# Performance work log

Hardware: AMD Instinct MI355X
Metric: run time of the kernel (lower is better)

Reference implementation:

```python
import jax, jax.numpy as jnp
import numpy as np

B, S = 1, 2048
D = 2048            # n_embd
H = 16              # num heads
KV = 4              # num kv heads
GROUPS = H // KV
D_NOPE = 128
D_ROPE = 64
D_QK = D_NOPE + D_ROPE   # 192
D_V = 128
Q_RANK = 1536
KV_RANK = 512
EPS = 1e-6
MAX_POS = 4096


def rms_norm(x, w, eps=EPS):
    x32 = x.astype(jnp.float32)
    y = x32 * jax.lax.rsqrt(jnp.mean(x32 * x32, axis=-1, keepdims=True) + eps)
    return y.astype(x.dtype) * w


def rotate_half(x):
    x1, x2 = jnp.split(x, 2, axis=-1)
    return jnp.concatenate((-x2, x1), axis=-1)


def setup_inputs() -> dict:
    key = jax.random.key(0)
    ks = jax.random.split(key, 10)
    inv_freq = 1.0 / (10000.0 ** (jnp.arange(0, D_ROPE, 2, dtype=jnp.float32) / D_ROPE))
    t = jnp.arange(MAX_POS, dtype=jnp.float32)
    freqs = jnp.outer(t, inv_freq)                      # [MAX_POS, D_ROPE//2]
    emb = jnp.concatenate((freqs, freqs), axis=-1)      # [MAX_POS, D_ROPE]
    def lin(k, fan_in, fan_out):
        return jax.random.normal(k, (fan_in, fan_out), dtype=jnp.float32) * (fan_in ** -0.5)
    return {
        "hidden_states": jax.random.normal(ks[0], (B, S, D), dtype=jnp.float32),
        "cos": jnp.cos(emb)[None],                      # [1, MAX_POS, D_ROPE]
        "sin": jnp.sin(emb)[None],
        "wq_a": lin(ks[1], D, Q_RANK),
        "q_a_ln_w": jnp.ones((Q_RANK,), jnp.float32),
        "wq_b": lin(ks[2], Q_RANK, H * D_QK),
        "wkv_a": lin(ks[3], D, KV_RANK + D_ROPE),
        "kv_a_ln_w": jnp.ones((KV_RANK,), jnp.float32),
        "wkv_b": lin(ks[4], KV_RANK, KV * (D_NOPE + D_V)),
        "wo": lin(ks[5], H * D_V, D),
        "cache_position": jnp.arange(S, dtype=jnp.int64),
    }


def reference(hidden_states, cos, sin, wq_a, q_a_ln_w, wq_b, wkv_a, kv_a_ln_w,
              wkv_b, wo, cache_position):
    b, s, _ = hidden_states.shape
    # --- query low-rank path ---
    q_a = hidden_states @ wq_a                           # [B,S,Q_RANK]
    q = rms_norm(q_a, q_a_ln_w) @ wq_b                   # [B,S,H*D_QK]
    q = q.reshape(b, s, H, D_QK).transpose(0, 2, 1, 3)   # [B,H,S,D_QK]
    q_pass, q_rot = q[..., :D_NOPE], q[..., D_NOPE:]
    # --- kv low-rank path ---
    ckv = hidden_states @ wkv_a                          # [B,S,KV_RANK+D_ROPE]
    k_pass_a, k_rot_a = ckv[..., :KV_RANK], ckv[..., KV_RANK:]
    kv = rms_norm(k_pass_a, kv_a_ln_w) @ wkv_b           # [B,S,KV*(D_NOPE+D_V)]
    kv = kv.reshape(b, s, KV, D_NOPE + D_V).transpose(0, 2, 1, 3)  # [B,KV,S,*]
    k_pass, v = kv[..., :D_NOPE], kv[..., D_NOPE:]
    # --- partial RoPE ---
    c = cos[0][cache_position][None, None]               # [1,1,S,D_ROPE]
    sn = sin[0][cache_position][None, None]
    q_rot = q_rot * c + rotate_half(q_rot) * sn          # [B,H,S,D_ROPE]
    k_rot = k_rot_a[:, None]                             # [B,1,S,D_ROPE]
    k_rot = k_rot * c + rotate_half(k_rot) * sn
    k_rot = jnp.broadcast_to(k_rot, (b, KV, s, D_ROPE))
    k = jnp.concatenate((k_pass, k_rot), axis=-1)        # [B,KV,S,D_QK]
    # GQA expansion (repeat_interleave over head dim)
    k = jnp.repeat(k, GROUPS, axis=1)                    # [B,H,S,D_QK]
    v = jnp.repeat(v, GROUPS, axis=1)                    # [B,H,S,D_V]
    q_full = jnp.concatenate((q_pass, q_rot), axis=-1)   # [B,H,S,D_QK]
    # causal SDPA (default scale = 1/sqrt(D_QK), matching torch sdpa)
    scale = 1.0 / jnp.sqrt(jnp.float32(D_QK))
    scores = jnp.einsum("bhqd,bhkd->bhqk", q_full, k) * scale
    causal = jnp.tril(jnp.ones((s, s), dtype=bool))
    scores = jnp.where(causal[None, None], scores, jnp.finfo(scores.dtype).min)
    attn = jax.nn.softmax(scores, axis=-1)
    out = jnp.einsum("bhqk,bhkd->bhqd", attn, v)         # [B,H,S,D_V]
    out = out.transpose(0, 2, 1, 3).reshape(b, s, H * D_V)
    return out @ wo                                      # [B,S,D]
```

## Files before the change

### kernel.cpp

```cpp
#include <hip/hip_runtime.h>
#include <hip/hip_bf16.h>


#define S_LEN 2048
#define D_MODEL 2048
#define NH 16
#define NKV 4
#define D_QK 192
#define D_NOPE 128
#define D_ROPE 64
#define D_V 128
#define Q_RANK 1536
#define KV_RANK 512
#define CKV_PITCH 640
#define QDIM (NH * D_QK)
#define KVDIM (NKV * (D_NOPE + D_V))
#define ODIM (NH * D_V)
#define SCALE_QK 0.07216878364870322f
#define SPLIT 2

#define DT_B16 0
#define DT_F32 1
#define DT_AUTO 2

typedef __bf16 bf16x8 __attribute__((ext_vector_type(8)));
typedef float  f32x4  __attribute__((ext_vector_type(4)));
typedef unsigned short u16x8 __attribute__((ext_vector_type(8)));

typedef __attribute__((address_space(1))) const unsigned int as1_u32;
typedef __attribute__((address_space(3))) unsigned int as3_u32;

__device__ __forceinline__ void gl2lds16(const unsigned short* g, unsigned short* l) {
    __builtin_amdgcn_global_load_lds((as1_u32*)g, (as3_u32*)l, 16, 0, 0);
}

__device__ __forceinline__ float b2f(unsigned short u) {
    return __uint_as_float(((unsigned int)u) << 16);
}
__device__ __forceinline__ unsigned short f2b(float f) {
    unsigned int u = __float_as_uint(f);
    return (unsigned short)((u + 0x7fffu + ((u >> 16) & 1u)) >> 16);
}
__device__ __forceinline__ bool flag_f32(const unsigned* dt) {
    return dt[0] == 0x3F800000u;
}
__device__ __forceinline__ bool eff_f32(int mode, bool f32) {
    return mode == DT_F32 || (mode == DT_AUTO && f32);
}
__device__ __forceinline__ float ldany(const void* p, size_t i, bool f32) {
    return f32 ? ((const float*)p)[i] : b2f(((const unsigned short*)p)[i]);
}

#if __has_builtin(__builtin_amdgcn_mov_dpp)
#define ROR16F(x, n) __int_as_float(__builtin_amdgcn_mov_dpp(__float_as_int(x), 0x120 + (n), 0xf, 0xf, true))
#else
#define ROR16F(x, n) __shfl_xor((x), (n))
#endif

__global__ void __launch_bounds__(256)
prep_k(const void* __restrict__ hs, unsigned short* __restrict__ hsb,
       const void* __restrict__ wq_a, unsigned short* __restrict__ wqaT,
       const void* __restrict__ wkv_a, unsigned short* __restrict__ wkvaT,
       const void* __restrict__ wq_b, unsigned short* __restrict__ wqbT,
       const void* __restrict__ wkv_b, unsigned short* __restrict__ wkvbT,
       const void* __restrict__ wo, unsigned short* __restrict__ woT,
       const unsigned* __restrict__ dt)
{
    const bool f32 = flag_f32(dt);
    const int t = threadIdx.x;
    int id = blockIdx.x;

    if (id < 1024) {
        const int base = id * 4096;
        for (int i = t; i < 4096; i += 256)
            hsb[base + i] = f2b(ldany(hs, base + i, f32));
        return;
    }
    id -= 1024;

    const void* W; unsigned short* WT; int Kdim, Ncols, nkb;
    if (id < 768)        { W = wq_a;  WT = wqaT;  Kdim = D_MODEL; Ncols = Q_RANK;           nkb = 32; }
    else if (id < 1088)  { id -= 768;  W = wkv_a; WT = wkvaT; Kdim = D_MODEL; Ncols = KV_RANK + D_ROPE; nkb = 32; }
    else if (id < 2240)  { id -= 1088; W = wq_b;  WT = wqbT;  Kdim = Q_RANK;  Ncols = QDIM;  nkb = 24; }
    else if (id < 2368)  { id -= 2240; W = wkv_b; WT = wkvbT; Kdim = KV_RANK; Ncols = KVDIM; nkb = 8;  }
    else                 { id -= 2368; W = wo;    WT = woT;   Kdim = ODIM;    Ncols = D_MODEL; nkb = 32; }

    const int k0 = (id % nkb) * 64, n0 = (id / nkb) * 64;

    __shared__ unsigned short tile[64][65];
    for (int i = t; i < 4096; i += 256) {
        int r = i >> 6, c = i & 63;
        float v = (n0 + c < Ncols) ? ldany(W, (size_t)(k0 + r) * Ncols + n0 + c, f32) : 0.f;
        tile[c][r] = f2b(v);
    }
    __syncthreads();
    for (int i = t; i < 4096; i += 256) {
        int nn = i >> 6, kk = i & 63;
        WT[(size_t)(n0 + nn) * Kdim + k0 + kk] = tile[nn][kk];
    }
}

#define SM(BUF, MAT, SUB) (smem + (((BUF) * 4 + (MAT) * 2 + (SUB)) * 4096))

__device__ __forceinline__ void
gemm_core(unsigned short* smem,
          const unsigned short* __restrict__ A, int lda,
          const unsigned short* __restrict__ BT, int ldb, int colB,
          void* __restrict__ C, int ldc, int colC, int K, bool cf, int row0)
{
    const int t = threadIdx.x;
    const int w = t >> 6, lane = t & 63;
    const int half = w >> 2;
    const int wq = w & 3;
    const int wr = wq & 1, wc = wq >> 1;
    const int n = lane & 15, quad = lane >> 4;
    const int e0 = t * 8;
    const int er = e0 >> 5, ec = e0 & 31;

    f32x4 acc[4][4];
#pragma unroll
    for (int i = 0; i < 4; ++i)
#pragma unroll
        for (int j = 0; j < 4; ++j) acc[i][j] = (f32x4){0.f, 0.f, 0.f, 0.f};

#define STAGE(BUF, KB)                                                         \
    do {                                                                       \
        gl2lds16(A  + (size_t)(row0 + er) * lda + (KB) + ec,                   \
                 SM(BUF, 0, 0) + e0);                                          \
        gl2lds16(A  + (size_t)(row0 + er) * lda + (KB) + 32 + ec,              \
                 SM(BUF, 0, 1) + e0);                                          \
        gl2lds16(BT + (size_t)(colB + er) * ldb + (KB) + ec,                   \
                 SM(BUF, 1, 0) + e0);                                          \
        gl2lds16(BT + (size_t)(colB + er) * ldb + (KB) + 32 + ec,              \
                 SM(BUF, 1, 1) + e0);                                          \
    } while (0)

    STAGE(0, 0);

    int cur = 0;
    for (int k0 = 0; k0 < K; k0 += 64) {
        __syncthreads();

        if (k0 + 64 < K) STAGE(cur ^ 1, k0 + 64);

        const unsigned short* Asub = SM(cur, 0, half);
        const unsigned short* Bsub = SM(cur, 1, half);

        bf16x8 af[4], bfr[4];
#pragma unroll
        for (int i = 0; i < 4; ++i)
            af[i] = *(const bf16x8*)&Asub[(wr * 64 + i * 16 + n) * 32 + quad * 8];
#pragma unroll
        for (int j = 0; j < 4; ++j)
            bfr[j] = *(const bf16x8*)&Bsub[(wc * 64 + j * 16 + n) * 32 + quad * 8];
#pragma unroll
        for (int i = 0; i < 4; ++i)
#pragma unroll
            for (int j = 0; j < 4; ++j)
                acc[i][j] = __builtin_amdgcn_mfma_f32_16x16x32_bf16(af[i], bfr[j], acc[i][j], 0, 0, 0);

        cur ^= 1;
    }
#undef STAGE

    __syncthreads();
    float* fsm = (float*)smem;
    if (half == 1) {
        float* dst = fsm + wq * 4096;
#pragma unroll
        for (int i = 0; i < 4; ++i)
#pragma unroll
            for (int j = 0; j < 4; ++j)
#pragma unroll
                for (int r = 0; r < 4; ++r)
                    dst[(i * 16 + quad * 4 + r) * 64 + j * 16 + n] = acc[i][j][r];
    }
    __syncthreads();
    if (half == 0) {
        const float* src = fsm + wq * 4096;
#pragma unroll
        for (int i = 0; i < 4; ++i)
#pragma unroll
            for (int j = 0; j < 4; ++j)
#pragma unroll
                for (int r = 0; r < 4; ++r)
                    acc[i][j][r] += src[(i * 16 + quad * 4 + r) * 64 + j * 16 + n];

#pragma unroll
        for (int i = 0; i < 4; ++i)
#pragma unroll
            for (int r = 0; r < 4; ++r) {
                const int row = row0 + wr * 64 + i * 16 + quad * 4 + r;
                if (cf) {
                    float* crow = (float*)C + (size_t)row * ldc + colC + wc * 64 + n;
#pragma unroll
                    for (int j = 0; j < 4; ++j) crow[j * 16] = acc[i][j][r];
                } else {
                    unsigned short* crow = (unsigned short*)C + (size_t)row * ldc + colC + wc * 64 + n;
#pragma unroll
                    for (int j = 0; j < 4; ++j) crow[j * 16] = f2b(acc[i][j][r]);
                }
            }
    }
}

__global__ void __launch_bounds__(512)
gemm_mfma(const unsigned short* __restrict__ A, int lda,
          const unsigned short* __restrict__ BT, int ldb,
          void* __restrict__ C, int ldc, int K, int cm,
          const unsigned* __restrict__ dt,
          void* __restrict__ C2, int ldc2, int ncol1)
{
    __shared__ unsigned short smem[2 * 2 * 2 * 4096];
    const int row0 = blockIdx.y << 7;
    const int colB = blockIdx.x << 7;
    void* Cp = C; int ld = ldc; int colC = colB;
    if (colC >= ncol1) { Cp = C2; ld = ldc2; colC -= ncol1; }
    const bool cf = eff_f32(cm, flag_f32(dt));
    gemm_core(smem, A, lda, BT, ldb, colB, Cp, ld, colC, K, cf, row0);
}

__global__ void __launch_bounds__(512)
gemm2_mfma(const unsigned short* __restrict__ A1, int lda1,
           const unsigned short* __restrict__ BT1, int ldb1,
           void* __restrict__ C1, int ldc1, int K1, int nbx1, int nblk1,
           const unsigned short* __restrict__ A2, int lda2,
           const unsigned short* __restrict__ BT2, int ldb2,
           void* __restrict__ C2, int ldc2, int K2, int nbx2)
{
    __shared__ unsigned short smem[2 * 2 * 2 * 4096];
    int id = blockIdx.x;
    if (id < nblk1) {
        const int bx = id % nbx1, by = id / nbx1;
        gemm_core(smem, A1, lda1, BT1, ldb1, bx << 7, C1, ldc1, bx << 7, K1, false, by << 7);
    } else {
        id -= nblk1;
        const int bx = id % nbx2, by = id / nbx2;
        gemm_core(smem, A2, lda2, BT2, ldb2, bx << 7, C2, ldc2, bx << 7, K2, false, by << 7);
    }
}

__global__ void __launch_bounds__(256)
rmsnorm2(unsigned short* __restrict__ qa, const void* __restrict__ qw,
         unsigned short* __restrict__ ckvb, const void* __restrict__ kw,
         const unsigned* __restrict__ dt)
{
    const bool f32 = flag_f32(dt);
    const int row = blockIdx.x;
    const int t = threadIdx.x;

    unsigned short* x;
    const void* w;
    int ncols;
    if (row < S_LEN) { x = qa + (size_t)row * Q_RANK; w = qw; ncols = Q_RANK; }
    else             { x = ckvb + (size_t)(row - S_LEN) * CKV_PITCH; w = kw; ncols = KV_RANK; }

    float ss = 0.f;
    for (int i = t; i < ncols; i += 256) { float v = b2f(x[i]); ss += v * v; }
#pragma unroll
    for (int o = 32; o > 0; o >>= 1) ss += __shfl_down(ss, o);

    __shared__ float part[4];
    __shared__ float sc;
    if ((t & 63) == 0) part[t >> 6] = ss;
    __syncthreads();
    if (t == 0) {
        float tot = part[0] + part[1] + part[2] + part[3];
        sc = rsqrtf(tot / (float)ncols + 1e-6f);
    }
    __syncthreads();
    float scale = sc;
    for (int i = t; i < ncols; i += 256)
        x[i] = f2b(b2f(x[i]) * scale * ldany(w, i, f32));
}

__global__ void __launch_bounds__(256)
rope_tv(unsigned short* __restrict__ q, unsigned short* __restrict__ ckvb,
        const void* __restrict__ cosb, const void* __restrict__ sinb,
        const void* __restrict__ cpos,
        const unsigned short* __restrict__ kvb, unsigned short* __restrict__ vt,
        const unsigned* __restrict__ dt)
{
    const int t = threadIdx.x;
    const int bid = blockIdx.x;

    if (bid < S_LEN) {
        const bool f32 = flag_f32(dt);
        const int s = bid;
        const long long* p64 = (const long long*)cpos;
        const int* p32 = (const int*)cpos;
        const bool is64 = (p64[1] == 1LL);
        const int pos = is64 ? (int)p64[s] : p32[s];
        const size_t cb = (size_t)pos * D_ROPE;

        for (int idx = t; idx < NH * 32; idx += 256) {
            int h = idx >> 5, i = idx & 31;
            unsigned short* base = q + (size_t)s * QDIM + h * D_QK + D_NOPE;
            float x1 = b2f(base[i]), x2 = b2f(base[i + 32]);
            float c1 = ldany(cosb, cb + i, f32),      s1 = ldany(sinb, cb + i, f32);
            float c2 = ldany(cosb, cb + i + 32, f32), s2 = ldany(sinb, cb + i + 32, f32);
            base[i]      = f2b(x1 * c1 - x2 * s1);
            base[i + 32] = f2b(x2 * c2 + x1 * s2);
        }
        if (t < 32) {
            int i = t;
            unsigned short* base = ckvb + (size_t)s * CKV_PITCH + KV_RANK;
            float x1 = b2f(base[i]), x2 = b2f(base[i + 32]);
            float c1 = ldany(cosb, cb + i, f32),      s1 = ldany(sinb, cb + i, f32);
            float c2 = ldany(cosb, cb + i + 32, f32), s2 = ldany(sinb, cb + i + 32, f32);
            base[i]      = f2b(x1 * c1 - x2 * s1);
            base[i + 32] = f2b(x2 * c2 + x1 * s2);
        }
        return;
    }

    __shared__ unsigned short tile[64][68];
    const int id2 = bid - S_LEN;
    const int kb = id2 & 31;
    const int yy = id2 >> 5;
    const int kvh = yy >> 1;
    const int d0 = (yy & 1) * 64;

    for (int i = t; i < 64 * 16; i += 256) {
        int r = i >> 4, c4 = (i & 15) << 2;
        ushort4 v = *(const ushort4*)(kvb + (size_t)(kb * 64 + r) * KVDIM
                                      + kvh * 256 + D_NOPE + d0 + c4);
        tile[c4 + 0][r] = v.x;
        tile[c4 + 1][r] = v.y;
        tile[c4 + 2][r] = v.z;
        tile[c4 + 3][r] = v.w;
    }
    __syncthreads();
    for (int i = t; i < 64 * 16; i += 256) {
        int d = i >> 4, k4 = (i & 15) << 2;
        ushort4 v = *(const ushort4*)&tile[d][k4];
        *(ushort4*)(vt + (size_t)(kvh * 128 + d0 + d) * S_LEN + kb * 64 + k4) = v;
    }
}

__global__ void __launch_bounds__(256, 2)
attn_mfma(const unsigned short* __restrict__ q, const unsigned short* __restrict__ kvb,
          const unsigned short* __restrict__ ckvb, const unsigned short* __restrict__ vt,
          unsigned short* __restrict__ pO, float* __restrict__ pm, float* __restrict__ pl)
{
    const int h   = blockIdx.y;
    const int qtb = (int)gridDim.x - 1 - (int)blockIdx.x;
    const int sp  = blockIdx.z;
    const int kvh = h >> 2;
    const int jtmax = 2 * qtb + 1;

    __shared__ unsigned short ks[64][200];
    __shared__ unsigned short vs[128][72];
    __shared__ unsigned short ps[4][2][16][72];

    const int t = threadIdx.x;
    const int w = t >> 6, lane = t & 63;
    const int n = lane & 15, quad = lane >> 4;
    const int qrow0 = qtb * 128 + w * 16;

    bf16x8 qf[2][6];
#pragma unroll
    for (int g = 0; g < 2; ++g) {
        const unsigned short* qrow = q + (size_t)(qrow0 + g * 64 + n) * QDIM + h * D_QK;
#pragma unroll
        for (int s = 0; s < 6; ++s)
            qf[g][s] = *(const bf16x8*)(qrow + s * 32 + quad * 8);
    }

    f32x4 o[2][8];
#pragma unroll
    for (int g = 0; g < 2; ++g)
#pragma unroll
        for (int c = 0; c < 8; ++c) o[g][c] = (f32x4){0.f, 0.f, 0.f, 0.f};
    float mrow[2][4], lrow[2][4];
#pragma unroll
    for (int g = 0; g < 2; ++g)
#pragma unroll
        for (int i = 0; i < 4; ++i) { mrow[g][i] = -3e38f; lrow[g][i] = 0.f; }

    u16x8 kn[4], kr[2], vv[4];

#define PRELOAD(K0)                                                            \
    {                                                                          \
        const int k0_ = (K0);                                                  \
        _Pragma("unroll")                                                      \
        for (int i = 0; i < 4; ++i) {                                          \
            int g = i * 256 + t, r = g >> 4, c = g & 15;                       \
            kn[i] = *(const u16x8*)(kvb + (size_t)(k0_ + r) * KVDIM            \
                                    + kvh * 256 + c * 8);                      \
        }                                                                      \
        _Pragma("unroll")                                                      \
        for (int i = 0; i < 2; ++i) {                                          \
            int g = i * 256 + t, r = g >> 3, c = g & 7;                        \
            kr[i] = *(const u16x8*)(ckvb + (size_t)(k0_ + r) * CKV_PITCH       \
                                    + KV_RANK + c * 8);                        \
        }                                                                      \
        _Pragma("unroll")                                                      \
        for (int i = 0; i < 4; ++i) {                                          \
            int g = i * 256 + t, d = g >> 3, c = g & 7;                        \
            vv[i] = *(const u16x8*)(vt + (size_t)(kvh * 128 + d) * S_LEN       \
                                    + k0_ + c * 8);                            \
        }                                                                      \
    }

    if (sp <= jtmax) PRELOAD(sp << 6);

    for (int jt = sp; jt <= jtmax; jt += SPLIT) {
        __syncthreads();
#pragma unroll
        for (int i = 0; i < 4; ++i) {
            int g = i * 256 + t, r = g >> 4, c = g & 15;
            *(u16x8*)&ks[r][c * 8] = kn[i];
        }
#pragma unroll
        for (int i = 0; i < 2; ++i) {
            int g = i * 256 + t, r = g >> 3, c = g & 7;
            *(u16x8*)&ks[r][128 + c * 8] = kr[i];
        }
#pragma unroll
        for (int i = 0; i < 4; ++i) {
            int g = i * 256 + t, d = g >> 3, c = g & 7;
            *(u16x8*)&vs[d][c * 8] = vv[i];
        }
        __syncthreads();

        if (jt + SPLIT <= jtmax) PRELOAD((jt + SPLIT) << 6);

        const bool act0  = (jt <= 2 * qtb);
        const bool diag0 = (jt == 2 * qtb);
        const bool diag1 = (jt == jtmax);

        f32x4 sf[2][4];
        __builtin_amdgcn_s_setprio(1);
#pragma unroll
        for (int f = 0; f < 4; ++f) {
            f32x4 a0 = (f32x4){0.f, 0.f, 0.f, 0.f};
            f32x4 a1 = (f32x4){0.f, 0.f, 0.f, 0.f};
#pragma unroll
            for (int s = 0; s < 6; ++s) {
                bf16x8 kf = *(const bf16x8*)&ks[f * 16 + n][s * 32 + quad * 8];
                a0 = __builtin_amdgcn_mfma_f32_16x16x32_bf16(qf[0][s], kf, a0, 0, 0, 0);
                a1 = __builtin_amdgcn_mfma_f32_16x16x32_bf16(qf[1][s], kf, a1, 0, 0, 0);
            }
            sf[0][f] = a0; sf[1][f] = a1;
        }
        __builtin_amdgcn_s_setprio(0);

        const bool actg[2]  = {act0, true};
        const bool diagg[2] = {diag0, diag1};

#pragma unroll
        for (int g = 0; g < 2; ++g) {
            if (!actg[g]) continue;
            const bool dg = diagg[g];
#pragma unroll
            for (int f = 0; f < 4; ++f)
#pragma unroll
                for (int i = 0; i < 4; ++i) {
                    float v = sf[g][f][i] * SCALE_QK;
                    if (dg && (f * 16 + n > w * 16 + quad * 4 + i)) v = -3e38f;
                    sf[g][f][i] = v;
                }

            float lmax[4], fac[4], alpha[4], lsum[4];
#pragma unroll
            for (int i = 0; i < 4; ++i)
                lmax[i] = fmaxf(fmaxf(fmaxf(sf[g][0][i], sf[g][1][i]),
                                      fmaxf(sf[g][2][i], sf[g][3][i])), mrow[g][i]);
#pragma unroll
            for (int f = 0; f < 4; ++f)
#pragma unroll
                for (int i = 0; i < 4; ++i)
                    sf[g][f][i] = __expf(sf[g][f][i] - lmax[i]);
#pragma unroll
            for (int i = 0; i < 4; ++i) {
                lsum[i] = (sf[g][0][i] + sf[g][1][i]) + (sf[g][2][i] + sf[g][3][i]);
                float gm = lmax[i];
                gm = fmaxf(gm, ROR16F(gm, 8));
                gm = fmaxf(gm, ROR16F(gm, 4));
                gm = fmaxf(gm, ROR16F(gm, 2));
                gm = fmaxf(gm, ROR16F(gm, 1));
                fac[i]   = __expf(lmax[i] - gm);
                alpha[i] = __expf(mrow[g][i] - gm);
                mrow[g][i] = gm;
                float s = lsum[i] * fac[i];
                s += ROR16F(s, 8);
                s += ROR16F(s, 4);
                s += ROR16F(s, 2);
                s += ROR16F(s, 1);
                lrow[g][i] = lrow[g][i] * alpha[i] + s;
#pragma unroll
                for (int c = 0; c < 8; ++c) o[g][c][i] *= alpha[i];
            }
#pragma unroll
            for (int f = 0; f < 4; ++f)
#pragma unroll
                for (int i = 0; i < 4; ++i)
                    ps[w][g][quad * 4 + i][f * 16 + n] = f2b(sf[g][f][i] * fac[i]);
        }

        __asm__ __volatile__("s_waitcnt lgkmcnt(0)" ::: "memory");

        bf16x8 pa[2][2];
#pragma unroll
        for (int g = 0; g < 2; ++g) {
            if (actg[g]) {
                pa[g][0] = *(const bf16x8*)&ps[w][g][n][quad * 8];
                pa[g][1] = *(const bf16x8*)&ps[w][g][n][32 + quad * 8];
            } else {
                pa[g][0] = (bf16x8)(__bf16)0.f;
                pa[g][1] = (bf16x8)(__bf16)0.f;
            }
        }

        __builtin_amdgcn_s_setprio(1);
#pragma unroll
        for (int c = 0; c < 8; ++c) {
            bf16x8 v0 = *(const bf16x8*)&vs[c * 16 + n][quad * 8];
            bf16x8 v1 = *(const bf16x8*)&vs[c * 16 + n][32 + quad * 8];
            o[0][c] = __builtin_amdgcn_mfma_f32_16x16x32_bf16(pa[0][0], v0, o[0][c], 0, 0, 0);
            o[0][c] = __builtin_amdgcn_mfma_f32_16x16x32_bf16(pa[0][1], v1, o[0][c], 0, 0, 0);
            o[1][c] = __builtin_amdgcn_mfma_f32_16x16x32_bf16(pa[1][0], v0, o[1][c], 0, 0, 0);
            o[1][c] = __builtin_amdgcn_mfma_f32_16x16x32_bf16(pa[1][1], v1, o[1][c], 0, 0, 0);
        }
        __builtin_amdgcn_s_setprio(0);
    }
#undef PRELOAD

#pragma unroll
    for (int g = 0; g < 2; ++g)
#pragma unroll
        for (int i = 0; i < 4; ++i) {
            const int row = qrow0 + g * 64 + quad * 4 + i;
            const size_t slot = ((size_t)(sp * S_LEN + row) * NH + h);
            unsigned short* orow = pO + slot * 128 + n;
#pragma unroll
            for (int c = 0; c < 8; ++c)
                orow[c * 16] = f2b(o[g][c][i]);
            if (n == 0) { pm[slot] = mrow[g][i]; pl[slot] = lrow[g][i]; }
        }
}

__global__ void __launch_bounds__(256)
combine_k(const unsigned short* __restrict__ pO, const float* __restrict__ pm,
          const float* __restrict__ pl, unsigned short* __restrict__ obuf)
{
    const int row = blockIdx.x;
    const int t = threadIdx.x;
    __shared__ float wsc[NH][SPLIT];

    if (t < NH) {
        const int h = t;
        float m[SPLIT], l[SPLIT];
        float mx = -3e38f;
#pragma unroll
        for (int s = 0; s < SPLIT; ++s) {
            const size_t slot = ((size_t)(s * S_LEN + row) * NH + h);
            m[s] = pm[slot]; l[s] = pl[slot];
            mx = fmaxf(mx, m[s]);
        }
        float lsum = 0.f;
#pragma unroll
        for (int s = 0; s < SPLIT; ++s) lsum += __expf(m[s] - mx) * l[s];
        float inv = 1.f / lsum;
#pragma unroll
        for (int s = 0; s < SPLIT; ++s) wsc[h][s] = __expf(m[s] - mx) * inv;
    }
    __syncthreads();

    for (int idx = t; idx < ODIM; idx += 256) {
        const int h = idx >> 7, d = idx & 127;
        float sum = 0.f;
#pragma unroll
        for (int s = 0; s < SPLIT; ++s) {
            const size_t slot = ((size_t)(s * S_LEN + row) * NH + h);
            sum += b2f(pO[slot * 128 + d]) * wsc[h][s];
        }
        obuf[(size_t)row * ODIM + idx] = f2b(sum);
    }
}


extern "C" void kernel_launch(void* const* d_in, const int* in_sizes, int n_in,
                              void* d_out, int out_size, void* d_ws, size_t ws_size,
                              hipStream_t stream)
{
    const void* hs    = d_in[0];
    const void* cosb  = d_in[1];
    const void* sinb  = d_in[2];
    const void* wq_a  = d_in[3];
    const void* q_ln  = d_in[4];
    const void* wq_b  = d_in[5];
    const void* wkv_a = d_in[6];
    const void* kv_ln = d_in[7];
    const void* wkv_b = d_in[8];
    const void* wo    = d_in[9];
    const void* cpos  = d_in[10];
    const unsigned* dt = (const unsigned*)d_in[4];

    char* ws = (char*)d_ws;
    unsigned short* woT   = (unsigned short*)ws; ws += (size_t)D_MODEL * ODIM    * 2;
    unsigned short* ckvb  = (unsigned short*)ws; ws += (size_t)S_LEN * CKV_PITCH * 2;
    unsigned short* qbuf  = (unsigned short*)ws; ws += (size_t)S_LEN * QDIM      * 2;
    unsigned short* kvb   = (unsigned short*)ws; ws += (size_t)S_LEN * KVDIM     * 2;
    unsigned short* vtb   = (unsigned short*)ws; ws += (size_t)NKV * D_V * S_LEN * 2;
    unsigned short* obuf  = (unsigned short*)ws; ws += (size_t)S_LEN * ODIM      * 2;

    char* scratch = ws;
    unsigned short* hsb   = (unsigned short*)scratch;
    unsigned short* wqaT  = hsb   + (size_t)S_LEN * D_MODEL;
    unsigned short* wkvaT = wqaT  + (size_t)Q_RANK * D_MODEL;
    unsigned short* wqbT  = wkvaT + (size_t)CKV_PITCH * D_MODEL;
    unsigned short* wkvbT = wqbT  + (size_t)QDIM * Q_RANK;
    unsigned short* q_a   = wkvbT + (size_t)KVDIM * KV_RANK;
    unsigned short* pO    = (unsigned short*)scratch;
    float*          pm    = (float*)(pO + (size_t)SPLIT * S_LEN * NH * 128);
    float*          pl    = pm + (size_t)SPLIT * S_LEN * NH;

    prep_k<<<4416, 256, 0, stream>>>(hs, hsb, wq_a, wqaT, wkv_a, wkvaT,
                                     wq_b, wqbT, wkv_b, wkvbT, wo, woT, dt);

    gemm_mfma<<<dim3((Q_RANK + CKV_PITCH) / 128, S_LEN / 128), 512, 0, stream>>>(
        hsb, D_MODEL, wqaT, D_MODEL, q_a, Q_RANK, D_MODEL, DT_B16, dt,
        ckvb, CKV_PITCH, Q_RANK);

    rmsnorm2<<<2 * S_LEN, 256, 0, stream>>>(q_a, q_ln, ckvb, kv_ln, dt);

    gemm2_mfma<<<(QDIM / 128) * (S_LEN / 128) + (KVDIM / 128) * (S_LEN / 128),
                 512, 0, stream>>>(
        q_a, Q_RANK, wqbT, Q_RANK, qbuf, QDIM, Q_RANK, QDIM / 128,
        (QDIM / 128) * (S_LEN / 128),
        ckvb, CKV_PITCH, wkvbT, KV_RANK, kvb, KVDIM, KV_RANK, KVDIM / 128);

    rope_tv<<<S_LEN + (S_LEN / 64) * 8, 256, 0, stream>>>(
        qbuf, ckvb, cosb, sinb, cpos, kvb, vtb, dt);

    attn_mfma<<<dim3(S_LEN / 128, NH, SPLIT), 256, 0, stream>>>(
        qbuf, kvb, ckvb, vtb, pO, pm, pl);

    combine_k<<<S_LEN, 256, 0, stream>>>(pO, pm, pl, obuf);

    gemm_mfma<<<dim3(D_MODEL / 128, S_LEN / 128), 512, 0, stream>>>(
        obuf, ODIM, woT, D_MODEL, d_out, D_MODEL, D_MODEL, DT_AUTO, dt,
        nullptr, 0, 1 << 30);
}
```

Baseline: 335.7 us.

## Triple-buffer GEMM LDS staging with vmcnt-based waits

Moves the MFMA GEMM core from double to triple buffering of A/B tiles in LDS, prefetching two k-steps ahead. Each step waits with s_waitcnt vmcnt only on the oldest stage, then issues a raw s_barrier. The goal is to hide more global-to-LDS load latency behind MFMA work. LDS per block grows from 64KB to 96KB, which may reduce occupancy.

Result: no change. 339.1 us (+1.0%).

```diff
diff --git a/kernel.cpp b/kernel.cpp
--- a/kernel.cpp
+++ b/kernel.cpp
@@ -100,7 +100,7 @@
     }
 }
 
-#define SM(BUF, MAT, SUB) (smem + (((BUF) * 4 + (MAT) * 2 + (SUB)) * 4096))
+#define SM3(SLOT, MAT, SUB) (smem + ((((SLOT) * 2 + (MAT)) * 2 + (SUB)) * 4096))
 
 __device__ __forceinline__ void
 gemm_core(unsigned short* smem,
@@ -123,43 +123,50 @@
 #pragma unroll
         for (int j = 0; j < 4; ++j) acc[i][j] = (f32x4){0.f, 0.f, 0.f, 0.f};
 
-#define STAGE(BUF, KB)                                                         \
+#define STAGE(SLOT, KB)                                                        \
     do {                                                                       \
         gl2lds16(A  + (size_t)(row0 + er) * lda + (KB) + ec,                   \
-                 SM(BUF, 0, 0) + e0);                                          \
+                 SM3(SLOT, 0, 0) + e0);                                        \
         gl2lds16(A  + (size_t)(row0 + er) * lda + (KB) + 32 + ec,              \
-                 SM(BUF, 0, 1) + e0);                                          \
+                 SM3(SLOT, 0, 1) + e0);                                        \
         gl2lds16(BT + (size_t)(colB + er) * ldb + (KB) + ec,                   \
-                 SM(BUF, 1, 0) + e0);                                          \
+                 SM3(SLOT, 1, 0) + e0);                                        \
         gl2lds16(BT + (size_t)(colB + er) * ldb + (KB) + 32 + ec,              \
-                 SM(BUF, 1, 1) + e0);                                          \
+                 SM3(SLOT, 1, 1) + e0);                                        \
     } while (0)
 
     STAGE(0, 0);
-
-    int cur = 0;
-    for (int k0 = 0; k0 < K; k0 += 64) {
-        __syncthreads();
-
-        if (k0 + 64 < K) STAGE(cur ^ 1, k0 + 64);
-
-        const unsigned short* Asub = SM(cur, 0, half);
-        const unsigned short* Bsub = SM(cur, 1, half);
+    STAGE(1, 64);
+
+    int s0 = 0, s1 = 1, s2 = 2;
+    const int nstep = K >> 6;
+    for (int i = 0; i < nstep; ++i) {
+        if (i + 1 < nstep) {
+            __asm__ __volatile__("s_waitcnt vmcnt(4)" ::: "memory");
+        } else {
+            __asm__ __volatile__("s_waitcnt vmcnt(0)" ::: "memory");
+        }
+        __builtin_amdgcn_s_barrier();
+
+        if (i + 2 < nstep) STAGE(s2, (i + 2) << 6);
+
+        const unsigned short* Asub = SM3(s0, 0, half);
+        const unsigned short* Bsub = SM3(s0, 1, half);
 
         bf16x8 af[4], bfr[4];
 #pragma unroll
-        for (int i = 0; i < 4; ++i)
-            af[i] = *(const bf16x8*)&Asub[(wr * 64 + i * 16 + n) * 32 + quad * 8];
+        for (int ii = 0; ii < 4; ++ii)
+            af[ii] = *(const bf16x8*)&Asub[(wr * 64 + ii * 16 + n) * 32 + quad * 8];
 #pragma unroll
         for (int j = 0; j < 4; ++j)
             bfr[j] = *(const bf16x8*)&Bsub[(wc * 64 + j * 16 + n) * 32 + quad * 8];
 #pragma unroll
-        for (int i = 0; i < 4; ++i)
+        for (int ii = 0; ii < 4; ++ii)
 #pragma unroll
             for (int j = 0; j < 4; ++j)
-                acc[i][j] = __builtin_amdgcn_mfma_f32_16x16x32_bf16(af[i], bfr[j], acc[i][j], 0, 0, 0);
-
-        cur ^= 1;
+                acc[ii][j] = __builtin_amdgcn_mfma_f32_16x16x32_bf16(af[ii], bfr[j], acc[ii][j], 0, 0, 0);
+
+        const int tmp = s0; s0 = s1; s1 = s2; s2 = tmp;
     }
 #undef STAGE
 
@@ -211,7 +218,7 @@
           const unsigned* __restrict__ dt,
           void* __restrict__ C2, int ldc2, int ncol1)
 {
-    __shared__ unsigned short smem[2 * 2 * 2 * 4096];
+    __shared__ unsigned short smem[3 * 2 * 2 * 4096];
     const int row0 = blockIdx.y << 7;
     const int colB = blockIdx.x << 7;
     void* Cp = C; int ld = ldc; int colC = colB;
@@ -228,7 +235,7 @@
            const unsigned short* __restrict__ BT2, int ldb2,
            void* __restrict__ C2, int ldc2, int K2, int nbx2)
 {
-    __shared__ unsigned short smem[2 * 2 * 2 * 4096];
+    __shared__ unsigned short smem[3 * 2 * 2 * 4096];
     int id = blockIdx.x;
     if (id < nblk1) {
         const int bx = id % nbx1, by = id / nbx1;
```
